# Kernel optimization log

Hardware: AMD Instinct MI355X
Metric: run time of the kernel (lower is better)

## Reference

```python
import jax, jax.numpy as jnp
import numpy as np

MUL = 64          # multiplicity of 0e and 1o channels
N_NODES = 50000
N_EDGES = 800000
NUM_NEIGHBORS = 16.0
SILU_NORM = 1.679177  # e3nn normalize2mom constant for silu


def setup_inputs() -> dict:
    key = jax.random.key(0)
    ks = jax.random.split(key, 9)
    node_in = jax.random.normal(ks[0], (N_NODES, 4 * MUL), dtype=jnp.float32)  # 64x0e + 64x1o
    edge_src = jax.random.randint(ks[1], (N_EDGES,), 0, N_NODES)
    edge_dst = jax.random.randint(ks[2], (N_EDGES,), 0, N_NODES)
    edge_attr = jax.random.normal(ks[3], (N_EDGES, 4), dtype=jnp.float32)      # 1x0e + 1x1o
    edge_len_emb = jax.random.uniform(ks[4], (N_EDGES, 10), dtype=jnp.float32)
    # tensor-product path weights [mul_in, mul_out] (mul_edge = 1)
    w_00_0 = jax.random.normal(ks[5], (MUL, MUL), dtype=jnp.float32)  # 0e x 0e -> 0e
    w_11_0 = jax.random.normal(ks[6], (MUL, MUL), dtype=jnp.float32)  # 1o x 1o -> 0e
    w_01_1 = jax.random.normal(ks[7], (MUL, MUL), dtype=jnp.float32)  # 0e x 1o -> 1o
    w_10_1 = jax.random.normal(ks[8], (MUL, MUL), dtype=jnp.float32)  # 1o x 0e -> 1o
    kf = jax.random.split(jax.random.fold_in(key, 1), 2)
    fc_w1 = jax.random.normal(kf[0], (10, 64), dtype=jnp.float32)
    fc_w2 = jax.random.normal(kf[1], (64, 1), dtype=jnp.float32)
    return {"node_in": node_in, "edge_attr": edge_attr, "edge_len_emb": edge_len_emb,
            "w_00_0": w_00_0, "w_11_0": w_11_0, "w_01_1": w_01_1, "w_10_1": w_10_1,
            "fc_w1": fc_w1, "fc_w2": fc_w2, "edge_src": edge_src, "edge_dst": edge_dst}


def reference(node_in, edge_attr, edge_len_emb, w_00_0, w_11_0, w_01_1, w_10_1,
              fc_w1, fc_w2, edge_src, edge_dst):
    # gather source node features per edge
    src = node_in[edge_src]                      # [E, 256]
    s0 = src[:, :MUL]                            # [E, mul]       scalars 0e
    s1 = src[:, MUL:].reshape(-1, MUL, 3)        # [E, mul, 3]    vectors 1o
    a0 = edge_attr[:, 0:1]                       # [E, 1]   edge 0e
    a1 = edge_attr[:, 1:4]                       # [E, 3]   edge 1o

    # fully-connected tensor product: path norm 1/sqrt(num_paths * fan_in)
    alpha = np.float32(1.0 / np.sqrt(2.0 * MUL))
    inv_sqrt3 = np.float32(1.0 / np.sqrt(3.0))
    # scalar output: 0e x 0e -> 0e  and  1o . 1o -> 0e (CG = delta/sqrt(3))
    out0 = alpha * (jnp.einsum('ei,io->eo', s0 * a0, w_00_0)
                    + inv_sqrt3 * jnp.einsum('eim,em,io->eo', s1, a1, w_11_0))   # [E, mul]
    # vector output: 0e x 1o -> 1o  and  1o x 0e -> 1o (CG = identity)
    out1 = alpha * (jnp.einsum('ei,io,em->eom', s0, w_01_1, a1)
                    + jnp.einsum('eim,io->eom', s1 * a0[:, :, None], w_10_1))     # [E, mul, 3]
    msg_ang = jnp.concatenate([out0, out1.reshape(-1, 3 * MUL)], axis=1)         # [E, 256]

    # radial MLP gate: FullyConnectedNet([10, 64, 1], silu)
    h = jax.nn.silu(edge_len_emb @ fc_w1 / np.float32(np.sqrt(10.0))) * np.float32(SILU_NORM)
    msg_rad = h @ fc_w2 / np.float32(np.sqrt(64.0))                              # [E, 1]

    messages = msg_ang * msg_rad
    agg = jax.ops.segment_sum(messages, edge_dst, num_segments=node_in.shape[0])
    return agg / np.float32(np.sqrt(NUM_NEIGHBORS))
```

## Files before the change

### kernel.cpp

```cpp
#include <hip/hip_runtime.h>

#define NE 800000
#define NN 50000
#define MAXD 60
#define FILL_BLK (NE / 256)
#define XC_BLK (NN / 8)

typedef __attribute__((ext_vector_type(4))) unsigned short ushort4v;
typedef __attribute__((ext_vector_type(4))) _Float16 f16x4;
typedef __attribute__((ext_vector_type(4))) float f32x4;

static constexpr float ALPHA      = 0.08838834764831845f;
static constexpr float INV3       = 0.57735026918962576f;
static constexpr float INV_SQRT10 = 0.31622776601683794f;
static constexpr float SILU_NORM  = 1.679177f;
static constexpr float QSCALE     = ALPHA * 0.25f;

__device__ __forceinline__ unsigned short f2h_bits(float f) {
  _Float16 h = (_Float16)f;
  unsigned short b;
  __builtin_memcpy(&b, &h, 2);
  return b;
}
__device__ __forceinline__ float h2f_bits(unsigned int b) {
  unsigned short s = (unsigned short)b;
  _Float16 h;
  __builtin_memcpy(&h, &s, 2);
  return (float)h;
}
__device__ __forceinline__ unsigned int packh2(float lo, float hi) {
  return (unsigned int)f2h_bits(lo) | ((unsigned int)f2h_bits(hi) << 16);
}

__global__ __launch_bounds__(256) void k_combo(
    const float* __restrict__ X, unsigned short* __restrict__ Xp,
    const float* __restrict__ attr, const float* __restrict__ emb,
    const float* __restrict__ w1, const float* __restrict__ w2,
    const int* __restrict__ esrc, const int* __restrict__ edst,
    int* __restrict__ cur, int* __restrict__ srcsE, uint2* __restrict__ sscalE) {
  __shared__ float lds[2816];
  if (blockIdx.x < FILL_BLK) {
    int eb = blockIdx.x * 256;
    const float* ebase = emb + (size_t)eb * 10;
#pragma unroll
    for (int j = 0; j < 10; j++)
      lds[j * 256 + threadIdx.x] = ebase[j * 256 + threadIdx.x];
    __syncthreads();
    const float* x = lds + threadIdx.x * 10;
    int e = eb + threadIdx.x;
    float r = 0.f;
#pragma unroll
    for (int j = 0; j < 64; j++) {
      float d = 0.f;
#pragma unroll
      for (int k = 0; k < 10; k++) d = fmaf(x[k], w1[k * 64 + j], d);
      d *= INV_SQRT10;
      float h = d * __builtin_amdgcn_rcpf(1.f + __expf(-d)) * SILU_NORM;
      r = fmaf(h, w2[j], r);
    }
    r *= 0.125f * QSCALE;
    float4 a = *(const float4*)(attr + (size_t)e * 4);
    int dst = edst[e];
    int slot = atomicAdd(&cur[dst], 1);
    if (slot < MAXD) {
      srcsE[dst * MAXD + slot] = esrc[e];
      sscalE[dst * MAXD + slot] =
          make_uint2(packh2(r * a.x, r * a.y), packh2(r * a.z, r * a.w));
    }
  } else {
    int n0 = (blockIdx.x - FILL_BLK) * 8;
    const float4* Xs = (const float4*)(X + (size_t)n0 * 256);
    float4* L4 = (float4*)lds;
    L4[threadIdx.x] = Xs[threadIdx.x];
    L4[256 + threadIdx.x] = Xs[256 + threadIdx.x];
    __syncthreads();
    int o = threadIdx.x & 63;
    int nl = threadIdx.x >> 6;
#pragma unroll
    for (int ii = 0; ii < 2; ii++) {
      int n_l = nl + ii * 4;
      const float* row = lds + n_l * 256;
      ushort4v v;
      v[0] = f2h_bits(row[o]);
      v[1] = f2h_bits(row[64 + 3 * o]);
      v[2] = f2h_bits(row[64 + 3 * o + 1]);
      v[3] = f2h_bits(row[64 + 3 * o + 2]);
      *(ushort4v*)(Xp + (size_t)(n0 + n_l) * 256 + o * 4) = v;
    }
  }
}

__device__ __forceinline__ void eop(uint2 p, ushort4v y, float& u0, float& u1,
                                    float& v0, float& v1, float& v2, float& w0,
                                    float& w1, float& w2) {
  float q0 = h2f_bits(p.x), q1 = h2f_bits(p.x >> 16);
  float q2 = h2f_bits(p.y), q3 = h2f_bits(p.y >> 16);
  float x0 = h2f_bits(y[0]), xa = h2f_bits(y[1]);
  float xb = h2f_bits(y[2]), xc = h2f_bits(y[3]);
  u0 = fmaf(q0, x0, u0);
  u1 = fmaf(q1, xa, u1);
  u1 = fmaf(q2, xb, u1);
  u1 = fmaf(q3, xc, u1);
  v0 = fmaf(q1, x0, v0);
  v1 = fmaf(q2, x0, v1);
  v2 = fmaf(q3, x0, v2);
  w0 = fmaf(q0, xa, w0);
  w1 = fmaf(q0, xb, w1);
  w2 = fmaf(q0, xc, w2);
}

__global__ __launch_bounds__(256) void k_agg(
    const int* __restrict__ cur, const int* __restrict__ srcsE,
    const uint2* __restrict__ sscalE, const unsigned short* __restrict__ Xp,
    unsigned short* __restrict__ P) {
  int n = blockIdx.x * 4 + (threadIdx.x >> 6);
  int o = threadIdx.x & 63;
  int d = cur[n];
  if (d > MAXD) d = MAXD;
  int base = n * MAXD;

  float u0 = 0.f, u1 = 0.f, v0 = 0.f, v1 = 0.f, v2 = 0.f;
  float w0 = 0.f, w1 = 0.f, w2 = 0.f;
  int i = 0;
  for (; i + 4 <= d; i += 4) {
    int s[4];
    uint2 p[4];
    ushort4v y[4];
#pragma unroll
    for (int q = 0; q < 4; q++) s[q] = srcsE[base + i + q];
#pragma unroll
    for (int q = 0; q < 4; q++) p[q] = sscalE[base + i + q];
#pragma unroll
    for (int q = 0; q < 4; q++)
      y[q] = *(const ushort4v*)(Xp + ((size_t)s[q] << 8) + (o << 2));
#pragma unroll
    for (int q = 0; q < 4; q++)
      eop(p[q], y[q], u0, u1, v0, v1, v2, w0, w1, w2);
  }
  for (; i < d; i++) {
    int s = srcsE[base + i];
    uint2 p = sscalE[base + i];
    ushort4v y = *(const ushort4v*)(Xp + ((size_t)s << 8) + (o << 2));
    eop(p, y, u0, u1, v0, v1, v2, w0, w1, w2);
  }

  size_t pb = (size_t)n * 512 + o;
  P[pb + 0 * 64] = f2h_bits(u0);
  P[pb + 1 * 64] = f2h_bits(u1 * INV3);
  P[pb + 2 * 64] = f2h_bits(v0);
  P[pb + 3 * 64] = f2h_bits(v1);
  P[pb + 4 * 64] = f2h_bits(v2);
  P[pb + 5 * 64] = f2h_bits(w0);
  P[pb + 6 * 64] = f2h_bits(w1);
  P[pb + 7 * 64] = f2h_bits(w2);
}

__global__ __launch_bounds__(256) void k_post(
    const unsigned short* __restrict__ P, const float* __restrict__ W00,
    const float* __restrict__ W11, const float* __restrict__ W01,
    const float* __restrict__ W10, float* __restrict__ out) {
  int l = threadIdx.x & 63;
  int lr = l & 15, lq = l >> 4;
  int tile = blockIdx.x * 4 + (threadIdx.x >> 6);
  int nb = tile * 16;
  if (nb >= NN) return;

  f16x4 a[8][4];
  const unsigned short* Pb = P + (size_t)(nb + lr) * 512;
#pragma unroll
  for (int c = 0; c < 8; c++) {
#pragma unroll
    for (int kq = 0; kq < 4; kq++) {
      ushort4v t = *(const ushort4v*)(Pb + c * 64 + kq * 16 + lq * 4);
      f16x4 af;
      __builtin_memcpy(&af, &t, 8);
      a[c][kq] = af;
    }
  }

#pragma unroll
  for (int j = 0; j < 4; j++) {
    int col = 16 * j + lr;
    f16x4 b00[4], b11[4], b01[4], b10[4];
#pragma unroll
    for (int kq = 0; kq < 4; kq++) {
#pragma unroll
      for (int i = 0; i < 4; i++) {
        int row = kq * 16 + lq * 4 + i;
        b00[kq][i] = (_Float16)W00[row * 64 + col];
        b11[kq][i] = (_Float16)W11[row * 64 + col];
        b01[kq][i] = (_Float16)W01[row * 64 + col];
        b10[kq][i] = (_Float16)W10[row * 64 + col];
      }
    }
    f32x4 acc0 = {0.f, 0.f, 0.f, 0.f};
#pragma unroll
    for (int kq = 0; kq < 4; kq++) {
      acc0 = __builtin_amdgcn_mfma_f32_16x16x16f16(a[0][kq], b00[kq], acc0, 0,
                                                   0, 0);
      acc0 = __builtin_amdgcn_mfma_f32_16x16x16f16(a[1][kq], b11[kq], acc0, 0,
                                                   0, 0);
    }
#pragma unroll
    for (int r = 0; r < 4; r++)
      out[(size_t)(nb + lq * 4 + r) * 256 + col] = acc0[r];
#pragma unroll
    for (int m = 0; m < 3; m++) {
      f32x4 acc = {0.f, 0.f, 0.f, 0.f};
#pragma unroll
      for (int kq = 0; kq < 4; kq++) {
        acc = __builtin_amdgcn_mfma_f32_16x16x16f16(a[2 + m][kq], b01[kq], acc,
                                                    0, 0, 0);
        acc = __builtin_amdgcn_mfma_f32_16x16x16f16(a[5 + m][kq], b10[kq], acc,
                                                    0, 0, 0);
      }
#pragma unroll
      for (int r = 0; r < 4; r++)
        out[(size_t)(nb + lq * 4 + r) * 256 + 64 + 3 * col + m] = acc[r];
    }
  }
}

extern "C" void kernel_launch(void* const* d_in, const int* in_sizes, int n_in,
                              void* d_out, int out_size, void* d_ws,
                              size_t ws_size, hipStream_t stream) {
  const float* node_in = (const float*)d_in[0];
  const float* edge_attr = (const float*)d_in[1];
  const float* emb = (const float*)d_in[2];
  const float* w00 = (const float*)d_in[3];
  const float* w11 = (const float*)d_in[4];
  const float* w01 = (const float*)d_in[5];
  const float* w10 = (const float*)d_in[6];
  const float* fw1 = (const float*)d_in[7];
  const float* fw2 = (const float*)d_in[8];
  const int* esrc = (const int*)d_in[9];
  const int* edst = (const int*)d_in[10];
  float* out = (float*)d_out;

  char* ws = (char*)d_ws;
  unsigned short* Xp = (unsigned short*)ws; ws += (size_t)NN * 256 * 2;
  unsigned short* P = (unsigned short*)ws;  ws += (size_t)NN * 512 * 2;
  int* srcsE = (int*)ws;                    ws += (size_t)NN * MAXD * 4;
  uint2* sscalE = (uint2*)ws;               ws += (size_t)NN * MAXD * 8;
  int* cur = (int*)ws;                      ws += (size_t)NN * 4;

  (void)hipMemsetAsync(cur, 0, (size_t)NN * 4, stream);
  k_combo<<<FILL_BLK + XC_BLK, 256, 0, stream>>>(
      node_in, Xp, edge_attr, emb, fw1, fw2, esrc, edst, cur, srcsE, sscalE);
  k_agg<<<NN / 4, 256, 0, stream>>>(cur, srcsE, sscalE, Xp, P);
  k_post<<<(NN / 16 + 3) / 4, 256, 0, stream>>>(P, w00, w11, w01, w10, out);
}
```

Baseline: 168.4 us.

## Fuse aggregation and MFMA post-projection via LDS, pack ELL records into uint4

Merges the per-node gather-aggregate kernel with the MFMA weight-projection kernel. Each 1024-thread block aggregates 16 nodes into a padded LDS tile, then its 16 waves each compute one output column block. This removes the global round trip of the fp16 intermediate P and one launch. Edge source index and packed scalars now share one 16-byte ELL record, so each edge needs a single load, and the atomic slot claim is moved before the radial MLP to hide its latency. MAXD grows to 64, which raises ELL memory. The 1024-thread blocks with launch_bounds(1024,1) may limit occupancy and latency hiding in the gather phase.

```diff
diff --git a/kernel.cpp b/kernel.cpp
--- a/kernel.cpp
+++ b/kernel.cpp
@@ -2,9 +2,10 @@
 
 #define NE 800000
 #define NN 50000
-#define MAXD 60
+#define MAXD 64
 #define FILL_BLK (NE / 256)
 #define XC_BLK (NN / 8)
+#define PSTR 516
 
 typedef __attribute__((ext_vector_type(4))) unsigned short ushort4v;
 typedef __attribute__((ext_vector_type(4))) _Float16 f16x4;
@@ -37,17 +38,22 @@
     const float* __restrict__ attr, const float* __restrict__ emb,
     const float* __restrict__ w1, const float* __restrict__ w2,
     const int* __restrict__ esrc, const int* __restrict__ edst,
-    int* __restrict__ cur, int* __restrict__ srcsE, uint2* __restrict__ sscalE) {
+    int* __restrict__ cur, uint4* __restrict__ ell) {
   __shared__ float lds[2816];
   if (blockIdx.x < FILL_BLK) {
     int eb = blockIdx.x * 256;
+    int e = eb + threadIdx.x;
+    int dst = edst[e];
+    int src = esrc[e];
+    float4 a = *(const float4*)(attr + (size_t)e * 4);
+    int slot = atomicAdd(&cur[dst], 1);
+
     const float* ebase = emb + (size_t)eb * 10;
 #pragma unroll
     for (int j = 0; j < 10; j++)
       lds[j * 256 + threadIdx.x] = ebase[j * 256 + threadIdx.x];
     __syncthreads();
     const float* x = lds + threadIdx.x * 10;
-    int e = eb + threadIdx.x;
     float r = 0.f;
 #pragma unroll
     for (int j = 0; j < 64; j++) {
@@ -59,13 +65,10 @@
       r = fmaf(h, w2[j], r);
     }
     r *= 0.125f * QSCALE;
-    float4 a = *(const float4*)(attr + (size_t)e * 4);
-    int dst = edst[e];
-    int slot = atomicAdd(&cur[dst], 1);
     if (slot < MAXD) {
-      srcsE[dst * MAXD + slot] = esrc[e];
-      sscalE[dst * MAXD + slot] =
-          make_uint2(packh2(r * a.x, r * a.y), packh2(r * a.z, r * a.w));
+      ell[dst * MAXD + slot] =
+          make_uint4((unsigned)src, packh2(r * a.x, r * a.y),
+                     packh2(r * a.z, r * a.w), 0u);
     }
   } else {
     int n0 = (blockIdx.x - FILL_BLK) * 8;
@@ -90,11 +93,12 @@
   }
 }
 
-__device__ __forceinline__ void eop(uint2 p, ushort4v y, float& u0, float& u1,
+__device__ __forceinline__ void eop(unsigned int q01, unsigned int q23,
+                                    ushort4v y, float& u0, float& u1,
                                     float& v0, float& v1, float& v2, float& w0,
                                     float& w1, float& w2) {
-  float q0 = h2f_bits(p.x), q1 = h2f_bits(p.x >> 16);
-  float q2 = h2f_bits(p.y), q3 = h2f_bits(p.y >> 16);
+  float q0 = h2f_bits(q01), q1 = h2f_bits(q01 >> 16);
+  float q2 = h2f_bits(q23), q3 = h2f_bits(q23 >> 16);
   float x0 = h2f_bits(y[0]), xa = h2f_bits(y[1]);
   float xb = h2f_bits(y[2]), xc = h2f_bits(y[3]);
   u0 = fmaf(q0, x0, u0);
@@ -109,115 +113,95 @@
   w2 = fmaf(q0, xc, w2);
 }
 
-__global__ __launch_bounds__(256) void k_agg(
-    const int* __restrict__ cur, const int* __restrict__ srcsE,
-    const uint2* __restrict__ sscalE, const unsigned short* __restrict__ Xp,
-    unsigned short* __restrict__ P) {
-  int n = blockIdx.x * 4 + (threadIdx.x >> 6);
+__global__ __launch_bounds__(1024, 1) void k_aggpost(
+    const int* __restrict__ cur, const uint4* __restrict__ ell,
+    const unsigned short* __restrict__ Xp, const float* __restrict__ W00,
+    const float* __restrict__ W11, const float* __restrict__ W01,
+    const float* __restrict__ W10, float* __restrict__ out) {
+  __shared__ unsigned short Pl[16 * PSTR];
+  int w = threadIdx.x >> 6;
   int o = threadIdx.x & 63;
+  int nb = blockIdx.x * 16;
+  int n = nb + w;
+
   int d = cur[n];
   if (d > MAXD) d = MAXD;
-  int base = n * MAXD;
+  const uint4* base = ell + n * MAXD;
 
   float u0 = 0.f, u1 = 0.f, v0 = 0.f, v1 = 0.f, v2 = 0.f;
   float w0 = 0.f, w1 = 0.f, w2 = 0.f;
   int i = 0;
   for (; i + 4 <= d; i += 4) {
-    int s[4];
-    uint2 p[4];
+    uint4 rec[4];
     ushort4v y[4];
 #pragma unroll
-    for (int q = 0; q < 4; q++) s[q] = srcsE[base + i + q];
-#pragma unroll
-    for (int q = 0; q < 4; q++) p[q] = sscalE[base + i + q];
+    for (int q = 0; q < 4; q++) rec[q] = base[i + q];
 #pragma unroll
     for (int q = 0; q < 4; q++)
-      y[q] = *(const ushort4v*)(Xp + ((size_t)s[q] << 8) + (o << 2));
+      y[q] = *(const ushort4v*)(Xp + ((size_t)rec[q].x << 8) + (o << 2));
 #pragma unroll
     for (int q = 0; q < 4; q++)
-      eop(p[q], y[q], u0, u1, v0, v1, v2, w0, w1, w2);
+      eop(rec[q].y, rec[q].z, y[q], u0, u1, v0, v1, v2, w0, w1, w2);
   }
   for (; i < d; i++) {
-    int s = srcsE[base + i];
-    uint2 p = sscalE[base + i];
-    ushort4v y = *(const ushort4v*)(Xp + ((size_t)s << 8) + (o << 2));
-    eop(p, y, u0, u1, v0, v1, v2, w0, w1, w2);
-  }
-
-  size_t pb = (size_t)n * 512 + o;
-  P[pb + 0 * 64] = f2h_bits(u0);
-  P[pb + 1 * 64] = f2h_bits(u1 * INV3);
-  P[pb + 2 * 64] = f2h_bits(v0);
-  P[pb + 3 * 64] = f2h_bits(v1);
-  P[pb + 4 * 64] = f2h_bits(v2);
-  P[pb + 5 * 64] = f2h_bits(w0);
-  P[pb + 6 * 64] = f2h_bits(w1);
-  P[pb + 7 * 64] = f2h_bits(w2);
-}
-
-__global__ __launch_bounds__(256) void k_post(
-    const unsigned short* __restrict__ P, const float* __restrict__ W00,
-    const float* __restrict__ W11, const float* __restrict__ W01,
-    const float* __restrict__ W10, float* __restrict__ out) {
-  int l = threadIdx.x & 63;
-  int lr = l & 15, lq = l >> 4;
-  int tile = blockIdx.x * 4 + (threadIdx.x >> 6);
-  int nb = tile * 16;
-  if (nb >= NN) return;
-
-  f16x4 a[8][4];
-  const unsigned short* Pb = P + (size_t)(nb + lr) * 512;
-#pragma unroll
-  for (int c = 0; c < 8; c++) {
-#pragma unroll
-    for (int kq = 0; kq < 4; kq++) {
-      ushort4v t = *(const ushort4v*)(Pb + c * 64 + kq * 16 + lq * 4);
-      f16x4 af;
-      __builtin_memcpy(&af, &t, 8);
-      a[c][kq] = af;
-    }
-  }
-
-#pragma unroll
-  for (int j = 0; j < 4; j++) {
-    int col = 16 * j + lr;
-    f16x4 b00[4], b11[4], b01[4], b10[4];
-#pragma unroll
-    for (int kq = 0; kq < 4; kq++) {
-#pragma unroll
-      for (int i = 0; i < 4; i++) {
-        int row = kq * 16 + lq * 4 + i;
-        b00[kq][i] = (_Float16)W00[row * 64 + col];
-        b11[kq][i] = (_Float16)W11[row * 64 + col];
-        b01[kq][i] = (_Float16)W01[row * 64 + col];
-        b10[kq][i] = (_Float16)W10[row * 64 + col];
-      }
-    }
-    f32x4 acc0 = {0.f, 0.f, 0.f, 0.f};
-#pragma unroll
-    for (int kq = 0; kq < 4; kq++) {
-      acc0 = __builtin_amdgcn_mfma_f32_16x16x16f16(a[0][kq], b00[kq], acc0, 0,
-                                                   0, 0);
-      acc0 = __builtin_amdgcn_mfma_f32_16x16x16f16(a[1][kq], b11[kq], acc0, 0,
-                                                   0, 0);
-    }
+    uint4 rec = base[i];
+    ushort4v y = *(const ushort4v*)(Xp + ((size_t)rec.x << 8) + (o << 2));
+    eop(rec.y, rec.z, y, u0, u1, v0, v1, v2, w0, w1, w2);
+  }
+
+  int rb = w * PSTR;
+  Pl[rb + 0 * 64 + o] = f2h_bits(u0);
+  Pl[rb + 1 * 64 + o] = f2h_bits(u1 * INV3);
+  Pl[rb + 2 * 64 + o] = f2h_bits(v0);
+  Pl[rb + 3 * 64 + o] = f2h_bits(v1);
+  Pl[rb + 4 * 64 + o] = f2h_bits(v2);
+  Pl[rb + 5 * 64 + o] = f2h_bits(w0);
+  Pl[rb + 6 * 64 + o] = f2h_bits(w1);
+  Pl[rb + 7 * 64 + o] = f2h_bits(w2);
+  __syncthreads();
+
+  int j = w & 3;
+  int part = w >> 2;
+  int lr = o & 15, lq = o >> 4;
+  int col = 16 * j + lr;
+
+  int c0 = (part == 0) ? 0 : 2 + (part - 1);
+  int c1 = (part == 0) ? 1 : 5 + (part - 1);
+  const float* Wp0 = (part == 0) ? W00 : W01;
+  const float* Wp1 = (part == 0) ? W11 : W10;
+
+  f16x4 a0[4], a1[4], b0[4], b1[4];
+#pragma unroll
+  for (int kq = 0; kq < 4; kq++) {
+    int od = kq * 16 + lq * 4;
+    ushort4v t0 = *(const ushort4v*)(Pl + lr * PSTR + c0 * 64 + od);
+    ushort4v t1 = *(const ushort4v*)(Pl + lr * PSTR + c1 * 64 + od);
+    __builtin_memcpy(&a0[kq], &t0, 8);
+    __builtin_memcpy(&a1[kq], &t1, 8);
+#pragma unroll
+    for (int ii = 0; ii < 4; ii++) {
+      int row = od + ii;
+      b0[kq][ii] = (_Float16)Wp0[row * 64 + col];
+      b1[kq][ii] = (_Float16)Wp1[row * 64 + col];
+    }
+  }
+
+  f32x4 acc = {0.f, 0.f, 0.f, 0.f};
+#pragma unroll
+  for (int kq = 0; kq < 4; kq++) {
+    acc = __builtin_amdgcn_mfma_f32_16x16x16f16(a0[kq], b0[kq], acc, 0, 0, 0);
+    acc = __builtin_amdgcn_mfma_f32_16x16x16f16(a1[kq], b1[kq], acc, 0, 0, 0);
+  }
+
+  if (part == 0) {
 #pragma unroll
     for (int r = 0; r < 4; r++)
-      out[(size_t)(nb + lq * 4 + r) * 256 + col] = acc0[r];
-#pragma unroll
-    for (int m = 0; m < 3; m++) {
-      f32x4 acc = {0.f, 0.f, 0.f, 0.f};
-#pragma unroll
-      for (int kq = 0; kq < 4; kq++) {
-        acc = __builtin_amdgcn_mfma_f32_16x16x16f16(a[2 + m][kq], b01[kq], acc,
-                                                    0, 0, 0);
-        acc = __builtin_amdgcn_mfma_f32_16x16x16f16(a[5 + m][kq], b10[kq], acc,
-                                                    0, 0, 0);
-      }
-#pragma unroll
-      for (int r = 0; r < 4; r++)
-        out[(size_t)(nb + lq * 4 + r) * 256 + 64 + 3 * col + m] = acc[r];
-    }
+      out[(size_t)(nb + lq * 4 + r) * 256 + col] = acc[r];
+  } else {
+    int m = part - 1;
+#pragma unroll
+    for (int r = 0; r < 4; r++)
+      out[(size_t)(nb + lq * 4 + r) * 256 + 64 + 3 * col + m] = acc[r];
   }
 }
 
@@ -239,14 +223,12 @@
 
   char* ws = (char*)d_ws;
   unsigned short* Xp = (unsigned short*)ws; ws += (size_t)NN * 256 * 2;
-  unsigned short* P = (unsigned short*)ws;  ws += (size_t)NN * 512 * 2;
-  int* srcsE = (int*)ws;                    ws += (size_t)NN * MAXD * 4;
-  uint2* sscalE = (uint2*)ws;               ws += (size_t)NN * MAXD * 8;
+  uint4* ell = (uint4*)ws;                  ws += (size_t)NN * MAXD * 16;
   int* cur = (int*)ws;                      ws += (size_t)NN * 4;
 
   (void)hipMemsetAsync(cur, 0, (size_t)NN * 4, stream);
   k_combo<<<FILL_BLK + XC_BLK, 256, 0, stream>>>(
-      node_in, Xp, edge_attr, emb, fw1, fw2, esrc, edst, cur, srcsE, sscalE);
-  k_agg<<<NN / 4, 256, 0, stream>>>(cur, srcsE, sscalE, Xp, P);
-  k_post<<<(NN / 16 + 3) / 4, 256, 0, stream>>>(P, w00, w11, w01, w10, out);
-}
+      node_in, Xp, edge_attr, emb, fw1, fw2, esrc, edst, cur, ell);
+  k_aggpost<<<NN / 16, 1024, 0, stream>>>(cur, ell, Xp, w00, w11, w01, w10,
+                                          out);
+}
```

New measurement: 145.9 us. -13.4%, faster.
